# Kernel tuning notes

Measured on AMD Instinct MI355X. Metric: run time of the kernel, lower is better.

Reference implementation:

```python
import jax, jax.numpy as jnp
import numpy as np

LEAK = 0.01   # nn.LeakyReLU default negative_slope
EPS = 1e-5    # BatchNorm eps

D, H, W = 32, 480, 480
N = 200000
CIN, COUT = 64, 128


def _neighbor_table(z, y, x, order, sorted_flat, offsets):
    # For each kernel offset, index of the active voxel at (z+dz, y+dy, x+dx), or -1.
    n = z.shape[0]
    tabs = []
    for dz, dy, dx in offsets:
        nz, ny, nx = z + dz, y + dy, x + dx
        valid = (nz >= 0) & (nz < D) & (ny >= 0) & (ny < H) & (nx >= 0) & (nx < W)
        nflat = (nz * H + ny) * W + nx
        pos = np.searchsorted(sorted_flat, nflat).clip(0, n - 1)
        found = valid & (sorted_flat[pos] == nflat)
        tabs.append(np.where(found, order[pos], -1).astype(np.int32))
    return np.stack(tabs)  # [9, N]


def setup_inputs() -> dict:
    rng = np.random.default_rng(0)
    flat = rng.choice(D * H * W, N, replace=False).astype(np.int64)
    z = flat // (H * W)
    y = (flat // W) % H
    x = flat % W
    order = np.argsort(flat)
    sorted_flat = flat[order]
    off133 = [(0, dy, dx) for dy in (-1, 0, 1) for dx in (-1, 0, 1)]  # kernel (1,3,3)
    off313 = [(dz, 0, dx) for dz in (-1, 0, 1) for dx in (-1, 0, 1)]  # kernel (3,1,3)
    nbr133 = jnp.asarray(_neighbor_table(z, y, x, order, sorted_flat, off133))
    nbr313 = jnp.asarray(_neighbor_table(z, y, x, order, sorted_flat, off313))

    key = jax.random.key(0)
    ks = jax.random.split(key, 14)
    feats = jax.random.normal(ks[0], (N, CIN), jnp.float32)
    # SubMConv3d weights, flattened kernel volume first: [9, Cin, Cout]
    W00 = jax.random.normal(ks[1], (9, CIN, COUT), jnp.float32) * 0.05   # conv0_0 (1,3,3)
    W01 = jax.random.normal(ks[2], (9, COUT, COUT), jnp.float32) * 0.05  # conv0_1 (3,1,3)
    W10 = jax.random.normal(ks[3], (9, CIN, COUT), jnp.float32) * 0.05   # conv1_0 (3,1,3)
    W11 = jax.random.normal(ks[4], (9, COUT, COUT), jnp.float32) * 0.05  # conv1_1 (1,3,3)

    def bn_params(k):
        k1, k2, k3, k4 = jax.random.split(k, 4)
        gamma = 1.0 + 0.1 * jax.random.normal(k1, (COUT,), jnp.float32)
        beta = 0.1 * jax.random.normal(k2, (COUT,), jnp.float32)
        mean = 0.1 * jax.random.normal(k3, (COUT,), jnp.float32)
        var = jax.random.uniform(k4, (COUT,), jnp.float32, 0.5, 1.5)
        return jnp.stack([gamma, beta, mean, var])  # [4, Cout]

    return {
        'feats': feats,
        'W00': W00, 'W01': W01, 'W10': W10, 'W11': W11,
        'bn00': bn_params(ks[5]), 'bn01': bn_params(ks[6]),
        'bn10': bn_params(ks[7]), 'bn11': bn_params(ks[8]),
        'nbr133': nbr133, 'nbr313': nbr313,
    }


def _subm_conv(f, nbr, Wk):
    # Rulebook gather-matmul-accumulate: out[n] = sum_k f[nbr[k, n]] @ Wk[k]
    out = jnp.zeros((f.shape[0], Wk.shape[2]), f.dtype)
    for k in range(Wk.shape[0]):  # 9 fixed kernel offsets
        idx = nbr[k]
        valid = idx >= 0
        g = jnp.where(valid[:, None], f[jnp.where(valid, idx, 0)], 0.0)
        out = out + g @ Wk[k]
    return out


def _act_bn(x, p):
    # LeakyReLU then BatchNorm (eval: running stats), matching forward order
    x = jnp.where(x >= 0, x, LEAK * x)
    scale = p[0] * jax.lax.rsqrt(p[3] + EPS)
    return (x - p[2]) * scale + p[1]


def reference(feats, W00, W01, W10, W11, bn00, bn01, bn10, bn11, nbr133, nbr313):
    shortcut = _act_bn(_subm_conv(feats, nbr133, W00), bn00)
    shortcut = _act_bn(_subm_conv(shortcut, nbr313, W01), bn01)
    res = _act_bn(_subm_conv(feats, nbr313, W10), bn10)
    res = _act_bn(_subm_conv(res, nbr133, W11), bn11)
    return res + shortcut
```

## Files before the change

kernel.cpp:

```cpp
#include <hip/hip_runtime.h>
#include <hip/hip_bf16.h>

#define LEAK 0.01f
#define BN_EPS 1e-5f
#define CAP_P 8192

using frag_b16 = __attribute__((ext_vector_type(8))) short;
using f32x4    = __attribute__((ext_vector_type(4))) float;

union U4F { uint4 u; frag_b16 f; };

__device__ __forceinline__ float bf2f(unsigned short u) {
    union { unsigned int i; float f; } v;
    v.i = ((unsigned int)u) << 16;
    return v.f;
}

__device__ __forceinline__ unsigned short f2bf(float f) {
    union { float f; unsigned int i; } v;
    v.f = f;
    unsigned int u = v.i;
    return (unsigned short)((u + 0x7fffu + ((u >> 16) & 1u)) >> 16);
}

__device__ __forceinline__ unsigned int pk_bf16(float lo, float hi) {
    __hip_bfloat162 h = __float22bfloat162_rn(make_float2(lo, hi));
    union { __hip_bfloat162 h; unsigned int u; } c;
    c.h = h;
    return c.u;
}

__global__ __launch_bounds__(256) void transpose_all(
    const float* __restrict__ w0, const float* __restrict__ w1,
    const float* __restrict__ w2, const float* __restrict__ w3,
    const float* __restrict__ b0, const float* __restrict__ b1,
    const float* __restrict__ b2, const float* __restrict__ b3,
    unsigned short* __restrict__ o0, unsigned short* __restrict__ o1,
    unsigned short* __restrict__ o2, unsigned short* __restrict__ o3,
    float* __restrict__ scsh) {
    const int t64 = 9 * 64 * 128, t128 = 9 * 128 * 128;
    int i = blockIdx.x * 256 + threadIdx.x;
    const float* w; unsigned short* o; int cin;
    if (i < t64)                        { w = w0; o = o0; cin = 64; }
    else if ((i -= t64) < t128)         { w = w1; o = o1; cin = 128; }
    else if ((i -= t128) < t64)         { w = w2; o = o2; cin = 64; }
    else if ((i -= t64) < t128)         { w = w3; o = o3; cin = 128; }
    else if ((i -= t128) < 512) {
        int conv = i >> 7, c = i & 127;
        const float* bn = (conv == 0) ? b0 : (conv == 1) ? b1 : (conv == 2) ? b2 : b3;
        float s = bn[c] * rsqrtf(bn[384 + c] + BN_EPS);
        scsh[conv * 256 + c] = s;
        scsh[conv * 256 + 128 + c] = bn[128 + c] - bn[256 + c] * s;
        return;
    }
    else return;
    int co = i & 127;
    int rest = i >> 7;
    int ci = rest % cin;
    int k = rest / cin;
    o[((size_t)k * 128 + co) * cin + ci] = f2bf(w[i]);
}

__global__ __launch_bounds__(256) void feats_to_bf16(
    const float* __restrict__ f, unsigned short* __restrict__ o, int total8) {
    int i = blockIdx.x * 256 + threadIdx.x;
    if (i >= total8) return;
    const float4* p4 = (const float4*)(f + (size_t)i * 8);
    float4 a = p4[0], b = p4[1];
    uint4 u;
    u.x = pk_bf16(a.x, a.y); u.y = pk_bf16(a.z, a.w);
    u.z = pk_bf16(b.x, b.y); u.w = pk_bf16(b.z, b.w);
    ((uint4*)o)[i] = u;
}

__global__ __launch_bounds__(256) void rules_count(
    const int* __restrict__ nbrA, const int* __restrict__ nbrB,
    int N, int NB, int* __restrict__ blockCnt) {
    __shared__ int cnts[16][4];
    const int tid = threadIdx.x, lane = tid & 63, wave = tid >> 6;
    const int n = blockIdx.x * 256 + tid;
    #pragma unroll
    for (int c = 0; c < 16; ++c) {
        const int* nb = (c < 8) ? nbrA : nbrB;
        int j = c & 7;
        int k = j + (j >= 4);
        int v = (n < N) ? nb[(size_t)k * N + n] : -1;
        unsigned long long m = __ballot(v >= 0);
        if (lane == 0) cnts[c][wave] = __popcll(m);
    }
    __syncthreads();
    if (tid < 16)
        blockCnt[tid * NB + blockIdx.x] =
            cnts[tid][0] + cnts[tid][1] + cnts[tid][2] + cnts[tid][3];
}

__global__ __launch_bounds__(1024) void rules_scan(
    const int* __restrict__ blockCnt, int NB,
    int* __restrict__ blockBase, int* __restrict__ meta) {
    const int lane = threadIdx.x & 63, w = threadIdx.x >> 6;
    int running = 0;
    for (int base = 0; base < NB; base += 64) {
        int i = base + lane;
        int v = (i < NB) ? blockCnt[w * NB + i] : 0;
        int s = v;
        #pragma unroll
        for (int d = 1; d < 64; d <<= 1) {
            int t = __shfl_up(s, d);
            if (lane >= d) s += t;
        }
        if (i < NB) blockBase[w * NB + i] = running + s - v;
        running += __shfl(s, 63);
    }
    if (lane == 0) meta[w] = running;
}

__global__ __launch_bounds__(256) void rules_fill(
    const int* __restrict__ nbrA, const int* __restrict__ nbrB,
    int N, int NB, const int* __restrict__ blockBase,
    int* __restrict__ pairsAll,
    int* __restrict__ ptabA, int* __restrict__ ptabB,
    uint4* __restrict__ pakA, uint4* __restrict__ pakB) {
    __shared__ int wcnt[16][4];
    __shared__ int wpre[16][4];
    const int tid = threadIdx.x, lane = tid & 63, wave = tid >> 6;
    const int n = blockIdx.x * 256 + tid;
    int vv[16], rk[16];
    #pragma unroll
    for (int c = 0; c < 16; ++c) {
        const int* nb = (c < 8) ? nbrA : nbrB;
        int j = c & 7;
        int k = j + (j >= 4);
        int v = (n < N) ? nb[(size_t)k * N + n] : -1;
        vv[c] = v;
        unsigned long long m = __ballot(v >= 0);
        rk[c] = (int)__popcll(m & ((1ull << lane) - 1ull));
        if (lane == 0) wcnt[c][wave] = (int)__popcll(m);
    }
    __syncthreads();
    if (tid < 16) {
        int s = 0;
        #pragma unroll
        for (int w = 0; w < 4; ++w) { wpre[tid][w] = s; s += wcnt[tid][w]; }
    }
    __syncthreads();
    if (n < N) {
        unsigned long long la0 = ~0ull, la1 = ~0ull, lb0 = ~0ull, lb1 = ~0ull;
        int na = 0, nbp = 0;
        #pragma unroll
        for (int c = 0; c < 16; ++c) {
            int j = c & 7;
            int idx = -1;
            if (vv[c] >= 0) {
                idx = blockBase[c * NB + blockIdx.x] + wpre[c][wave] + rk[c];
                if (idx < CAP_P) pairsAll[c * CAP_P + idx] = vv[c];
                else idx = -1;
            }
            if (c < 8) { if (ptabA) ptabA[(size_t)n * 8 + j] = idx; }
            else       { if (ptabB) ptabB[(size_t)n * 8 + j] = idx; }
            if (idx >= 0) {
                unsigned e = ((unsigned)j << 13) | (unsigned)idx;
                if (e != 0xFFFFu) {
                    if (c < 8) {
                        int s = (na & 3) * 16;
                        unsigned long long m = 0xFFFFull << s;
                        unsigned long long ev = (unsigned long long)e << s;
                        if (na < 4) la0 = (la0 & ~m) | ev; else la1 = (la1 & ~m) | ev;
                        ++na;
                    } else {
                        int s = (nbp & 3) * 16;
                        unsigned long long m = 0xFFFFull << s;
                        unsigned long long ev = (unsigned long long)e << s;
                        if (nbp < 4) lb0 = (lb0 & ~m) | ev; else lb1 = (lb1 & ~m) | ev;
                        ++nbp;
                    }
                }
            }
        }
        if (pakA) pakA[n] = make_uint4((unsigned)la0, (unsigned)(la0 >> 32),
                                       (unsigned)la1, (unsigned)(la1 >> 32));
        if (pakB) pakB[n] = make_uint4((unsigned)lb0, (unsigned)(lb0 >> 32),
                                       (unsigned)lb1, (unsigned)(lb1 >> 32));
    }
}


__device__ __forceinline__ void merge_gather4(
    uint4 pk, const unsigned short* __restrict__ contrib, int cOff, f32x4 (&acc)[4]) {
    if (pk.x == 0xFFFFFFFFu) return;
    unsigned long long lo = ((unsigned long long)pk.y << 32) | pk.x;
    unsigned long long hi = ((unsigned long long)pk.w << 32) | pk.z;
    #pragma unroll 1
    for (int t = 0; t < 8; ++t) {
        unsigned v = (unsigned)(((t < 4) ? lo : hi) >> ((t & 3) << 4)) & 0xFFFFu;
        if (v == 0xFFFFu) break;
        const unsigned short* cr =
            contrib + ((size_t)(v >> 13) * CAP_P + (v & 0x1FFFu)) * 128 + cOff;
        #pragma unroll
        for (int ni = 0; ni < 4; ++ni) {
            uint2 g = *(const uint2*)(cr + ni * 16);
            acc[ni][0] += bf2f((unsigned short)(g.x & 0xffffu));
            acc[ni][1] += bf2f((unsigned short)(g.x >> 16));
            acc[ni][2] += bf2f((unsigned short)(g.y & 0xffffu));
            acc[ni][3] += bf2f((unsigned short)(g.y >> 16));
        }
    }
}

template <int CIN, bool IN_F32>
__global__ __launch_bounds__(256) void pairs_fused(
    const void* __restrict__ finA, const void* __restrict__ finB,
    const int*  __restrict__ pairsAll,
    const int*  __restrict__ meta,
    const unsigned short* __restrict__ wtA,
    const unsigned short* __restrict__ wtB,
    unsigned short* __restrict__ contribLo,
    unsigned short* __restrict__ contribHi,
    int pairXor) {
    const int job = blockIdx.y;
    const int j = job & 7, k = j + (j >= 4);
    const bool second = job >= 8;
    const void* fin = second ? finB : finA;
    const unsigned short* wk = (second ? wtB : wtA) + (size_t)k * 128 * CIN;
    unsigned short* ctb = (second ? contribHi : contribLo) + (size_t)j * CAP_P * 128;
    const int pidx = job ^ pairXor;
    const int* pairs = pairsAll + (size_t)pidx * CAP_P;
    const int cnt = min(meta[pidx], CAP_P);
    const int wave = threadIdx.x >> 6, lane = threadIdx.x & 63;
    const int l16 = lane & 15, quad = lane >> 4;
    const int pbase = (blockIdx.x * 4 + wave) * 16;
    if (pbase >= cnt) return;
    const int p = pbase + l16;
    const int inrow = (p < cnt) ? pairs[p] : -1;

    U4F uIn[CIN / 32];
    #pragma unroll
    for (int c = 0; c < CIN / 32; ++c) {
        uIn[c].u = make_uint4(0u, 0u, 0u, 0u);
        if (inrow >= 0) {
            if (IN_F32) {
                const float* fp = (const float*)fin;
                const float4* p4 = (const float4*)(fp + (size_t)inrow * CIN + c * 32 + quad * 8);
                float4 a = p4[0], b = p4[1];
                uIn[c].u.x = pk_bf16(a.x, a.y); uIn[c].u.y = pk_bf16(a.z, a.w);
                uIn[c].u.z = pk_bf16(b.x, b.y); uIn[c].u.w = pk_bf16(b.z, b.w);
            } else {
                uIn[c].u = *(const uint4*)((const unsigned short*)fin + (size_t)inrow * CIN + c * 32 + quad * 8);
            }
        }
    }

    f32x4 acc[8] = {};
    #pragma unroll
    for (int c = 0; c < CIN / 32; ++c) {
        frag_b16 bfr = uIn[c].f;
        #pragma unroll
        for (int ni = 0; ni < 8; ++ni) {
            frag_b16 afr = *(const frag_b16*)(wk + (size_t)(ni * 16 + l16) * CIN + c * 32 + quad * 8);
            acc[ni] = __builtin_amdgcn_mfma_f32_16x16x32_bf16(afr, bfr, acc[ni], 0, 0, 0);
        }
    }
    if (p < cnt) {
        unsigned short* cr = ctb + (size_t)p * 128 + quad * 4;
        #pragma unroll
        for (int ni = 0; ni < 8; ++ni) {
            uint2 o;
            o.x = pk_bf16(acc[ni][0], acc[ni][1]);
            o.y = pk_bf16(acc[ni][2], acc[ni][3]);
            *(uint2*)(cr + ni * 16) = o;
        }
    }
}

template <bool IN_F32>
__global__ __launch_bounds__(256) void convK1(
    const void* __restrict__ feats_,
    const unsigned short* __restrict__ wt00,
    const unsigned short* __restrict__ wt10,
    const uint4* __restrict__ pakA,
    const uint4* __restrict__ pakB,
    const unsigned short* __restrict__ contribLo,
    const unsigned short* __restrict__ contribHi,
    const float* __restrict__ scsh,
    unsigned short* __restrict__ s1,
    unsigned short* __restrict__ r1,
    int N) {
    constexpr int CIN = 64, SEGS = 8;
    __shared__ unsigned short ldsS[128 * CIN];
    __shared__ unsigned short ldsR[128 * CIN];
    const int tid = threadIdx.x, lane = tid & 63, wave = tid >> 6;
    const int waveM = wave >> 1, waveN = wave & 1;
    const int l16 = lane & 15, quad = lane >> 4;
    const int n0 = blockIdx.x * 64;
    {
        const unsigned short* wS = wt00 + (size_t)4 * 128 * CIN;
        const unsigned short* wR = wt10 + (size_t)4 * 128 * CIN;
        #pragma unroll
        for (int g = 0; g < (128 * SEGS) / 256; ++g) {
            int idx = g * 256 + tid;
            int row = idx / SEGS, seg = idx % SEGS;
            int dst = row * CIN + ((seg ^ (row & 7)) << 3);
            *(uint4*)(ldsS + dst) = *(const uint4*)(wS + row * CIN + seg * 8);
            *(uint4*)(ldsR + dst) = *(const uint4*)(wR + row * CIN + seg * 8);
        }
    }

    U4F bF[2][2];
    uint4 pA[2], pB[2];
    #pragma unroll
    for (int mi = 0; mi < 2; ++mi) {
        int n = n0 + waveM * 32 + mi * 16 + l16;
        pA[mi] = make_uint4(~0u, ~0u, ~0u, ~0u);
        pB[mi] = pA[mi];
        #pragma unroll
        for (int c = 0; c < 2; ++c) bF[c][mi].u = make_uint4(0u, 0u, 0u, 0u);
        if (n < N) {
            if (IN_F32) {
                const float* fp = (const float*)feats_;
                #pragma unroll
                for (int c = 0; c < 2; ++c) {
                    const float4* p4 = (const float4*)(fp + (size_t)n * 64 + c * 32 + quad * 8);
                    float4 a = p4[0], b = p4[1];
                    bF[c][mi].u.x = pk_bf16(a.x, a.y); bF[c][mi].u.y = pk_bf16(a.z, a.w);
                    bF[c][mi].u.z = pk_bf16(b.x, b.y); bF[c][mi].u.w = pk_bf16(b.z, b.w);
                }
            } else {
                #pragma unroll
                for (int c = 0; c < 2; ++c)
                    bF[c][mi].u = *(const uint4*)((const unsigned short*)feats_ + (size_t)n * 64 + c * 32 + quad * 8);
            }
            pA[mi] = pakA[n];
            pB[mi] = pakB[n];
        }
    }
    __syncthreads();

    f32x4 accS[2][4] = {}, accR[2][4] = {};
    #pragma unroll
    for (int c = 0; c < 2; ++c) {
        #pragma unroll
        for (int ni = 0; ni < 4; ++ni) {
            int off = (waveN * 64 + ni * 16 + l16) * CIN + ((((c << 2) + quad) ^ (l16 & 7)) << 3);
            frag_b16 aS = *(const frag_b16*)(ldsS + off);
            frag_b16 aR = *(const frag_b16*)(ldsR + off);
            #pragma unroll
            for (int mi = 0; mi < 2; ++mi) {
                accS[mi][ni] = __builtin_amdgcn_mfma_f32_16x16x32_bf16(aS, bF[c][mi].f, accS[mi][ni], 0, 0, 0);
                accR[mi][ni] = __builtin_amdgcn_mfma_f32_16x16x32_bf16(aR, bF[c][mi].f, accR[mi][ni], 0, 0, 0);
            }
        }
    }

    const int cOff = waveN * 64 + quad * 4;
    #pragma unroll
    for (int mi = 0; mi < 2; ++mi) {
        int n = n0 + waveM * 32 + mi * 16 + l16;
        if (n >= N) continue;
        merge_gather4(pA[mi], contribLo, cOff, accS[mi]);
        merge_gather4(pB[mi], contribHi, cOff, accR[mi]);
        #pragma unroll
        for (int ni = 0; ni < 4; ++ni) {
            int c = cOff + ni * 16;
            f32x4 scS = *(const f32x4*)(scsh + c);
            f32x4 shS = *(const f32x4*)(scsh + 128 + c);
            f32x4 scR = *(const f32x4*)(scsh + 512 + c);
            f32x4 shR = *(const f32x4*)(scsh + 640 + c);
            float vs[4], vr[4];
            #pragma unroll
            for (int r = 0; r < 4; ++r) {
                float xs = accS[mi][ni][r];
                xs = (xs >= 0.0f) ? xs : LEAK * xs;
                vs[r] = xs * scS[r] + shS[r];
                float xr = accR[mi][ni][r];
                xr = (xr >= 0.0f) ? xr : LEAK * xr;
                vr[r] = xr * scR[r] + shR[r];
            }
            uint2 oS, oR;
            oS.x = pk_bf16(vs[0], vs[1]); oS.y = pk_bf16(vs[2], vs[3]);
            oR.x = pk_bf16(vr[0], vr[1]); oR.y = pk_bf16(vr[2], vr[3]);
            *(uint2*)(s1 + (size_t)n * 128 + c) = oS;
            *(uint2*)(r1 + (size_t)n * 128 + c) = oR;
        }
    }
}

__global__ __launch_bounds__(256) void convK2(
    const unsigned short* __restrict__ s1,
    const unsigned short* __restrict__ r1,
    const unsigned short* __restrict__ wt01,
    const unsigned short* __restrict__ wt11,
    const uint4* __restrict__ pakB,
    const uint4* __restrict__ pakA,
    const unsigned short* __restrict__ contribLo,
    const unsigned short* __restrict__ contribHi,
    const float* __restrict__ scsh,
    float* __restrict__ out, int N) {
    constexpr int CIN = 128, SEGS = 16;
    __shared__ unsigned short ldsS[128 * CIN];
    __shared__ unsigned short ldsR[128 * CIN];
    const int tid = threadIdx.x, lane = tid & 63, wave = tid >> 6;
    const int waveM = wave >> 1, waveN = wave & 1;
    const int l16 = lane & 15, quad = lane >> 4;
    const int n0 = blockIdx.x * 64;
    {
        const unsigned short* wS = wt01 + (size_t)4 * 128 * CIN;
        const unsigned short* wR = wt11 + (size_t)4 * 128 * CIN;
        #pragma unroll
        for (int g = 0; g < (128 * SEGS) / 256; ++g) {
            int idx = g * 256 + tid;
            int row = idx >> 4, seg = idx & 15;
            int dst = row * CIN + ((seg ^ (row & 7)) << 3);
            *(uint4*)(ldsS + dst) = *(const uint4*)(wS + row * CIN + seg * 8);
            *(uint4*)(ldsR + dst) = *(const uint4*)(wR + row * CIN + seg * 8);
        }
    }

    U4F bS[4][2], bR[4][2];
    uint4 pS[2], pR[2];
    #pragma unroll
    for (int mi = 0; mi < 2; ++mi) {
        int n = n0 + waveM * 32 + mi * 16 + l16;
        pS[mi] = make_uint4(~0u, ~0u, ~0u, ~0u);
        pR[mi] = pS[mi];
        #pragma unroll
        for (int c = 0; c < 4; ++c) {
            bS[c][mi].u = make_uint4(0u, 0u, 0u, 0u);
            bR[c][mi].u = bS[c][mi].u;
        }
        if (n < N) {
            #pragma unroll
            for (int c = 0; c < 4; ++c) {
                bS[c][mi].u = *(const uint4*)(s1 + (size_t)n * 128 + c * 32 + quad * 8);
                bR[c][mi].u = *(const uint4*)(r1 + (size_t)n * 128 + c * 32 + quad * 8);
            }
            pS[mi] = pakB[n];
            pR[mi] = pakA[n];
        }
    }
    __syncthreads();

    f32x4 accS[2][4] = {}, accR[2][4] = {};
    #pragma unroll
    for (int c = 0; c < 4; ++c) {
        #pragma unroll
        for (int ni = 0; ni < 4; ++ni) {
            int off = (waveN * 64 + ni * 16 + l16) * CIN + ((((c << 2) + quad) ^ (l16 & 7)) << 3);
            frag_b16 aS = *(const frag_b16*)(ldsS + off);
            frag_b16 aR = *(const frag_b16*)(ldsR + off);
            #pragma unroll
            for (int mi = 0; mi < 2; ++mi) {
                accS[mi][ni] = __builtin_amdgcn_mfma_f32_16x16x32_bf16(aS, bS[c][mi].f, accS[mi][ni], 0, 0, 0);
                accR[mi][ni] = __builtin_amdgcn_mfma_f32_16x16x32_bf16(aR, bR[c][mi].f, accR[mi][ni], 0, 0, 0);
            }
        }
    }

    const int cOff = waveN * 64 + quad * 4;
    #pragma unroll
    for (int mi = 0; mi < 2; ++mi) {
        int n = n0 + waveM * 32 + mi * 16 + l16;
        if (n >= N) continue;
        merge_gather4(pS[mi], contribLo, cOff, accS[mi]);
        merge_gather4(pR[mi], contribHi, cOff, accR[mi]);
        #pragma unroll
        for (int ni = 0; ni < 4; ++ni) {
            int c = cOff + ni * 16;
            f32x4 sc1 = *(const f32x4*)(scsh + 256 + c);
            f32x4 sh1 = *(const f32x4*)(scsh + 384 + c);
            f32x4 sc3 = *(const f32x4*)(scsh + 768 + c);
            f32x4 sh3 = *(const f32x4*)(scsh + 896 + c);
            f32x4 o;
            #pragma unroll
            for (int r = 0; r < 4; ++r) {
                float xs = accS[mi][ni][r];
                xs = (xs >= 0.0f) ? xs : LEAK * xs;
                xs = xs * sc1[r] + sh1[r];
                float xr = accR[mi][ni][r];
                xr = (xr >= 0.0f) ? xr : LEAK * xr;
                xr = xr * sc3[r] + sh3[r];
                o[r] = xr + xs;
            }
            *(f32x4*)(out + (size_t)n * 128 + c) = o;
        }
    }
}


template <int CIN, bool IN_F32>
__global__ __launch_bounds__(256) void pairs_gemm2(
    const void* __restrict__ fin_,
    const int*  __restrict__ pairsT,
    const int*  __restrict__ metaT,
    const unsigned short* __restrict__ wt,
    unsigned short* __restrict__ contrib) {
    const int j = blockIdx.y;
    const int k = j + (j >= 4);
    const int cnt = min(metaT[j], CAP_P);
    const int wave = threadIdx.x >> 6, lane = threadIdx.x & 63;
    const int base = (blockIdx.x * 4 + wave) * 16;
    if (base >= cnt) return;
    const int l16 = lane & 15, quad = lane >> 4;
    const int p = base + l16;
    const int inrow = (p < cnt) ? pairsT[j * CAP_P + p] : -1;
    const unsigned short* wk = wt + (size_t)k * 128 * CIN;

    f32x4 acc[8] = {};
    #pragma unroll
    for (int c = 0; c < CIN / 32; ++c) {
        U4F u;
        u.u = make_uint4(0u, 0u, 0u, 0u);
        if (inrow >= 0) {
            if (IN_F32) {
                const float* fin = (const float*)fin_;
                const float4* p4 = (const float4*)(fin + (size_t)inrow * CIN + c * 32 + quad * 8);
                float4 a = p4[0], b = p4[1];
                u.u.x = pk_bf16(a.x, a.y); u.u.y = pk_bf16(a.z, a.w);
                u.u.z = pk_bf16(b.x, b.y); u.u.w = pk_bf16(b.z, b.w);
            } else {
                u.u = *(const uint4*)((const unsigned short*)fin_ + (size_t)inrow * CIN + c * 32 + quad * 8);
            }
        }
        frag_b16 af = u.f;
        #pragma unroll
        for (int ni = 0; ni < 8; ++ni) {
            frag_b16 bf = *(const frag_b16*)(wk + (ni * 16 + l16) * CIN + c * 32 + quad * 8);
            acc[ni] = __builtin_amdgcn_mfma_f32_16x16x32_bf16(af, bf, acc[ni], 0, 0, 0);
        }
    }
    unsigned short* cj = contrib + ((size_t)j * CAP_P + base) * 128;
    #pragma unroll
    for (int r = 0; r < 4; ++r) {
        int row = quad * 4 + r;
        #pragma unroll
        for (int ni = 0; ni < 8; ++ni)
            cj[(size_t)row * 128 + ni * 16 + l16] = f2bf(acc[ni][r]);
    }
}

template <int CIN, bool IN_F32, bool OUT_BF16, int ADDMODE>
__global__ __launch_bounds__(256, 4) void conv_center3(
    const void* __restrict__ fin_,
    const unsigned short* __restrict__ wt,
    const int*  __restrict__ ptabT,
    const unsigned short* __restrict__ contrib,
    const float* __restrict__ bn,
    const unsigned short* __restrict__ addbf,
    void* __restrict__ out_,
    int N) {
    const int tid = threadIdx.x;
    const int lane = tid & 63;
    const int wave = tid >> 6;
    const int waveM = wave >> 1, waveN = wave & 1;
    const int l16 = lane & 15, quad = lane >> 4;
    const int n0 = blockIdx.x * 64;
    const unsigned short* wc = wt + (size_t)4 * 128 * CIN;

    f32x4 acc[2][4] = {};
    #pragma unroll
    for (int c = 0; c < CIN / 32; ++c) {
        frag_b16 bf[4], af[2];
        #pragma unroll
        for (int ni = 0; ni < 4; ++ni)
            bf[ni] = *(const frag_b16*)(wc + (waveN * 64 + ni * 16 + l16) * CIN + c * 32 + quad * 8);
        #pragma unroll
        for (int mi = 0; mi < 2; ++mi) {
            int n = n0 + waveM * 32 + mi * 16 + l16;
            U4F u;
            u.u = make_uint4(0u, 0u, 0u, 0u);
            if (n < N) {
                if (IN_F32) {
                    const float* fin = (const float*)fin_;
                    const float4* p4 = (const float4*)(fin + (size_t)n * CIN + c * 32 + quad * 8);
                    float4 a = p4[0], b = p4[1];
                    u.u.x = pk_bf16(a.x, a.y); u.u.y = pk_bf16(a.z, a.w);
                    u.u.z = pk_bf16(b.x, b.y); u.u.w = pk_bf16(b.z, b.w);
                } else {
                    u.u = *(const uint4*)((const unsigned short*)fin_ + (size_t)n * CIN + c * 32 + quad * 8);
                }
            }
            af[mi] = u.f;
        }
        #pragma unroll
        for (int mi = 0; mi < 2; ++mi)
            #pragma unroll
            for (int ni = 0; ni < 4; ++ni)
                acc[mi][ni] = __builtin_amdgcn_mfma_f32_16x16x32_bf16(af[mi], bf[ni], acc[mi][ni], 0, 0, 0);
    }

    float sc[4], sh[4];
    int col[4];
    #pragma unroll
    for (int ni = 0; ni < 4; ++ni) {
        int c = waveN * 64 + ni * 16 + l16;
        col[ni] = c;
        float s = bn[c] * rsqrtf(bn[384 + c] + BN_EPS);
        sc[ni] = s;
        sh[ni] = bn[128 + c] - bn[256 + c] * s;
    }
    #pragma unroll
    for (int mi = 0; mi < 2; ++mi) {
        int rbase = n0 + waveM * 32 + mi * 16 + quad * 4;
        #pragma unroll
        for (int r = 0; r < 4; ++r) {
            int n = rbase + r;
            if (n < N) {
                const int4* pt = (const int4*)(ptabT + (size_t)n * 8);
                int4 pa = pt[0], pb = pt[1];
                int pj[8] = {pa.x, pa.y, pa.z, pa.w, pb.x, pb.y, pb.z, pb.w};
                float m[4] = {0.f, 0.f, 0.f, 0.f};
                #pragma unroll
                for (int j = 0; j < 8; ++j) {
                    int pi = pj[j];
                    if (pi >= 0) {
                        const unsigned short* cr = contrib + ((size_t)j * CAP_P + pi) * 128;
                        #pragma unroll
                        for (int ni = 0; ni < 4; ++ni) m[ni] += bf2f(cr[col[ni]]);
                    }
                }
                float addv[4] = {0.f, 0.f, 0.f, 0.f};
                if (ADDMODE == 1) {
                    #pragma unroll
                    for (int ni = 0; ni < 4; ++ni)
                        addv[ni] = bf2f(addbf[(size_t)n * 128 + col[ni]]);
                } else if (ADDMODE == 2) {
                    #pragma unroll
                    for (int ni = 0; ni < 4; ++ni)
                        addv[ni] = ((const float*)out_)[(size_t)n * 128 + col[ni]];
                }
                #pragma unroll
                for (int ni = 0; ni < 4; ++ni) {
                    float x = acc[mi][ni][r] + m[ni];
                    x = (x >= 0.0f) ? x : LEAK * x;
                    x = x * sc[ni] + sh[ni];
                    x += addv[ni];
                    if (OUT_BF16)
                        ((unsigned short*)out_)[(size_t)n * 128 + col[ni]] = f2bf(x);
                    else
                        ((float*)out_)[(size_t)n * 128 + col[ni]] = x;
                }
            }
        }
    }
}

template <int CIN, bool IN_F32, bool OUT_F32, bool ADD>
__global__ __launch_bounds__(256) void conv_mfma(
    const void*  __restrict__ fin_,
    const int*   __restrict__ nbr,
    const unsigned short* __restrict__ wt,
    const float* __restrict__ bn,
    const float* __restrict__ addsrc,
    void*        __restrict__ out_,
    int N) {
    constexpr int SEGS = CIN / 8;
    constexpr int RPP = 256 / SEGS;
    constexpr int PASSES = 128 / RPP;
    __shared__ unsigned short ldsA[128 * CIN];
    __shared__ unsigned short ldsW[128 * CIN];
    const int tid = threadIdx.x;
    const int lane = tid & 63;
    const int wave = tid >> 6;
    const int waveM = wave >> 1, waveN = wave & 1;
    const int l16 = lane & 15, quad = lane >> 4;
    const int n0 = blockIdx.x * 128;
    const int srow = tid / SEGS, sseg = tid % SEGS;
    f32x4 acc[4][4] = {};
    for (int k = 0; k < 9; ++k) {
        if (k) __syncthreads();
        #pragma unroll
        for (int p = 0; p < PASSES; ++p) {
            int r = p * RPP + srow;
            int n = n0 + r;
            int idx = (n < N) ? nbr[(size_t)k * N + n] : -1;
            uint4 v = make_uint4(0u, 0u, 0u, 0u);
            if (IN_F32) {
                const float* fin = (const float*)fin_;
                float4 a = make_float4(0.f, 0.f, 0.f, 0.f);
                float4 b = make_float4(0.f, 0.f, 0.f, 0.f);
                if (idx >= 0) {
                    const float4* p4 = (const float4*)(fin + (size_t)idx * CIN) + sseg * 2;
                    a = p4[0]; b = p4[1];
                }
                v.x = pk_bf16(a.x, a.y); v.y = pk_bf16(a.z, a.w);
                v.z = pk_bf16(b.x, b.y); v.w = pk_bf16(b.z, b.w);
            } else {
                const unsigned short* fin = (const unsigned short*)fin_;
                if (idx >= 0) v = *((const uint4*)(fin + (size_t)idx * CIN) + sseg);
            }
            *(uint4*)(ldsA + r * CIN + ((sseg ^ (r & 7)) << 3)) = v;
        }
        const unsigned short* wk = wt + (size_t)k * 128 * CIN;
        #pragma unroll
        for (int p = 0; p < PASSES; ++p) {
            int r = p * RPP + srow;
            *(uint4*)(ldsW + r * CIN + ((sseg ^ (r & 7)) << 3)) =
                *((const uint4*)(wk + r * CIN) + sseg);
        }
        __syncthreads();
        #pragma unroll
        for (int c = 0; c < CIN / 32; ++c) {
            frag_b16 af[4], bf[4];
            #pragma unroll
            for (int i = 0; i < 4; ++i) {
                int seg = (c * 4 + quad) ^ (l16 & 7);
                af[i] = *(const frag_b16*)(ldsA + (waveM * 64 + i * 16 + l16) * CIN + (seg << 3));
                bf[i] = *(const frag_b16*)(ldsW + (waveN * 64 + i * 16 + l16) * CIN + (seg << 3));
            }
            #pragma unroll
            for (int mi = 0; mi < 4; ++mi)
                #pragma unroll
                for (int ni = 0; ni < 4; ++ni)
                    acc[mi][ni] = __builtin_amdgcn_mfma_f32_16x16x32_bf16(af[mi], bf[ni], acc[mi][ni], 0, 0, 0);
        }
    }
    float sc[4], sh[4];
    int col[4];
    #pragma unroll
    for (int ni = 0; ni < 4; ++ni) {
        int c = waveN * 64 + ni * 16 + l16;
        col[ni] = c;
        float s = bn[c] * rsqrtf(bn[384 + c] + BN_EPS);
        sc[ni] = s;
        sh[ni] = bn[128 + c] - bn[256 + c] * s;
    }
    #pragma unroll
    for (int mi = 0; mi < 4; ++mi) {
        int rbase = n0 + waveM * 64 + mi * 16 + quad * 4;
        #pragma unroll
        for (int r = 0; r < 4; ++r) {
            int n = rbase + r;
            if (n < N) {
                #pragma unroll
                for (int ni = 0; ni < 4; ++ni) {
                    float x = acc[mi][ni][r];
                    x = (x >= 0.0f) ? x : LEAK * x;
                    x = x * sc[ni] + sh[ni];
                    if (ADD) x += addsrc[(size_t)n * 128 + col[ni]];
                    if (OUT_F32) ((float*)out_)[(size_t)n * 128 + col[ni]] = x;
                    else ((unsigned short*)out_)[(size_t)n * 128 + col[ni]] = f2bf(x);
                }
            }
        }
    }
}

extern "C" void kernel_launch(void* const* d_in, const int* in_sizes, int n_in,
                              void* d_out, int out_size, void* d_ws, size_t ws_size,
                              hipStream_t stream) {
    const float* feats = (const float*)d_in[0];
    const float* W00 = (const float*)d_in[1];
    const float* W01 = (const float*)d_in[2];
    const float* W10 = (const float*)d_in[3];
    const float* W11 = (const float*)d_in[4];
    const float* bn00 = (const float*)d_in[5];
    const float* bn01 = (const float*)d_in[6];
    const float* bn10 = (const float*)d_in[7];
    const float* bn11 = (const float*)d_in[8];
    const int* nbr133 = (const int*)d_in[9];
    const int* nbr313 = (const int*)d_in[10];
    const int N = in_sizes[0] / 64;
    const int NB = (N + 255) / 256;

    char* ws = (char*)d_ws;
    size_t off = 0;
    auto alloc = [&](size_t bytes) -> char* {
        char* p = ws + off;
        off = (off + bytes + 255) & ~(size_t)255;
        return p;
    };
    unsigned short* bufA = (unsigned short*)alloc((size_t)N * 128 * 2);
    unsigned short* wt00 = (unsigned short*)alloc(9 * 128 * 64 * 2);
    unsigned short* wt01 = (unsigned short*)alloc(9 * 128 * 128 * 2);
    unsigned short* wt10 = (unsigned short*)alloc(9 * 128 * 64 * 2);
    unsigned short* wt11 = (unsigned short*)alloc(9 * 128 * 128 * 2);
    float* scsh = (float*)alloc(4 * 2 * 128 * 4);
    int* pairsAll = (int*)alloc((size_t)16 * CAP_P * 4);
    int* blockCnt = (int*)alloc((size_t)16 * NB * 4);
    int* blockBase = (int*)alloc((size_t)16 * NB * 4);
    int* meta = (int*)alloc(16 * 4);
    unsigned short* contribLo = (unsigned short*)alloc((size_t)8 * CAP_P * 128 * 2);
    const size_t offX = off;

    uint4* pakA = (uint4*)alloc((size_t)N * 16);
    uint4* pakB = (uint4*)alloc((size_t)N * 16);
    unsigned short* bufB = (unsigned short*)alloc((size_t)N * 128 * 2);
    unsigned short* contribHi = (unsigned short*)alloc((size_t)8 * CAP_P * 128 * 2);
    const size_t offFused = off;
    unsigned short* feats16 = (unsigned short*)alloc((size_t)N * 64 * 2);
    const size_t offFusedF16 = off;

    off = offX;
    int* ptab133 = (int*)alloc((size_t)N * 8 * 4);
    int* ptab313 = (int*)alloc((size_t)N * 8 * 4);
    const size_t offTierB = off;
    unsigned short* bufB_t = (unsigned short*)alloc((size_t)N * 128 * 2);
    const size_t offTierA = off;

    const bool fusedOk = (ws_size >= offFused);
    const bool useF16 = (ws_size >= offFusedF16);
    const bool tierA = (ws_size >= offTierA);
    const bool tierB = (ws_size >= offTierB);

    const int totalW = 2 * (9 * 64 * 128) + 2 * (9 * 128 * 128);
    hipLaunchKernelGGL(transpose_all, dim3((totalW + 512 + 255) / 256), dim3(256), 0, stream,
                       W00, W01, W10, W11, bn00, bn01, bn10, bn11,
                       wt00, wt01, wt10, wt11, scsh);

    float* outF = (float*)d_out;
    const int cblocks = (N + 63) / 64;

    if (fusedOk) {
        if (useF16) {
            const int total8 = N * 8;
            hipLaunchKernelGGL(feats_to_bf16, dim3((total8 + 255) / 256), dim3(256), 0, stream,
                               feats, feats16, total8);
        }
        hipLaunchKernelGGL(rules_count, dim3(NB), dim3(256), 0, stream,
                           nbr133, nbr313, N, NB, blockCnt);
        hipLaunchKernelGGL(rules_scan, dim3(1), dim3(1024), 0, stream,
                           blockCnt, NB, blockBase, meta);
        hipLaunchKernelGGL(rules_fill, dim3(NB), dim3(256), 0, stream,
                           nbr133, nbr313, N, NB, blockBase, pairsAll,
                           (int*)nullptr, (int*)nullptr, pakA, pakB);

        const dim3 pg(CAP_P / 64, 16);
        if (useF16) {
            hipLaunchKernelGGL((pairs_fused<64, false>), pg, dim3(256), 0, stream,
                               (const void*)feats16, (const void*)feats16, pairsAll, meta,
                               wt00, wt10, contribLo, contribHi, 0);
            hipLaunchKernelGGL((convK1<false>), dim3(cblocks), dim3(256), 0, stream,
                               (const void*)feats16, wt00, wt10, pakA, pakB,
                               contribLo, contribHi, scsh, bufA, bufB, N);
        } else {
            hipLaunchKernelGGL((pairs_fused<64, true>), pg, dim3(256), 0, stream,
                               (const void*)feats, (const void*)feats, pairsAll, meta,
                               wt00, wt10, contribLo, contribHi, 0);
            hipLaunchKernelGGL((convK1<true>), dim3(cblocks), dim3(256), 0, stream,
                               (const void*)feats, wt00, wt10, pakA, pakB,
                               contribLo, contribHi, scsh, bufA, bufB, N);
        }
        hipLaunchKernelGGL((pairs_fused<128, false>), pg, dim3(256), 0, stream,
                           (const void*)bufA, (const void*)bufB, pairsAll, meta,
                           wt01, wt11, contribLo, contribHi, 8);
        hipLaunchKernelGGL(convK2, dim3(cblocks), dim3(256), 0, stream,
                           bufA, bufB, wt01, wt11, pakB, pakA,
                           contribLo, contribHi, scsh, outF, N);
    } else if (tierA || tierB) {
        hipLaunchKernelGGL(rules_count, dim3(NB), dim3(256), 0, stream,
                           nbr133, nbr313, N, NB, blockCnt);
        hipLaunchKernelGGL(rules_scan, dim3(1), dim3(1024), 0, stream,
                           blockCnt, NB, blockBase, meta);
        hipLaunchKernelGGL(rules_fill, dim3(NB), dim3(256), 0, stream,
                           nbr133, nbr313, N, NB, blockBase, pairsAll,
                           ptab133, ptab313, (uint4*)nullptr, (uint4*)nullptr);

        const dim3 pg(CAP_P / 64, 8);
        const int* pairs133 = pairsAll;
        const int* pairs313 = pairsAll + 8 * CAP_P;
        const int* meta133 = meta;
        const int* meta313 = meta + 8;
        const unsigned short* nullbf = nullptr;

        hipLaunchKernelGGL((pairs_gemm2<64, true>), pg, dim3(256), 0, stream,
                           (const void*)feats, pairs133, meta133, wt00, contribLo);
        hipLaunchKernelGGL((conv_center3<64, true, true, 0>), dim3(cblocks), dim3(256), 0, stream,
                           (const void*)feats, wt00, ptab133, contribLo, bn00, nullbf, (void*)bufA, N);
        hipLaunchKernelGGL((pairs_gemm2<128, false>), pg, dim3(256), 0, stream,
                           (const void*)bufA, pairs313, meta313, wt01, contribLo);
        if (tierA)
            hipLaunchKernelGGL((conv_center3<128, false, true, 0>), dim3(cblocks), dim3(256), 0, stream,
                               (const void*)bufA, wt01, ptab313, contribLo, bn01, nullbf, (void*)bufB_t, N);
        else
            hipLaunchKernelGGL((conv_center3<128, false, false, 0>), dim3(cblocks), dim3(256), 0, stream,
                               (const void*)bufA, wt01, ptab313, contribLo, bn01, nullbf, (void*)outF, N);
        hipLaunchKernelGGL((pairs_gemm2<64, true>), pg, dim3(256), 0, stream,
                           (const void*)feats, pairs313, meta313, wt10, contribLo);
        hipLaunchKernelGGL((conv_center3<64, true, true, 0>), dim3(cblocks), dim3(256), 0, stream,
                           (const void*)feats, wt10, ptab313, contribLo, bn10, nullbf, (void*)bufA, N);
        hipLaunchKernelGGL((pairs_gemm2<128, false>), pg, dim3(256), 0, stream,
                           (const void*)bufA, pairs133, meta133, wt11, contribLo);
        if (tierA)
            hipLaunchKernelGGL((conv_center3<128, false, false, 1>), dim3(cblocks), dim3(256), 0, stream,
                               (const void*)bufA, wt11, ptab133, contribLo, bn11, bufB_t, (void*)outF, N);
        else
            hipLaunchKernelGGL((conv_center3<128, false, false, 2>), dim3(cblocks), dim3(256), 0, stream,
                               (const void*)bufA, wt11, ptab133, contribLo, bn11, nullbf, (void*)outF, N);
    } else {
        const int blocks = (N + 127) / 128;
        hipLaunchKernelGGL((conv_mfma<64, true, false, false>), dim3(blocks), dim3(256), 0, stream,
                           (const void*)feats, nbr133, wt00, bn00, (const float*)nullptr, (void*)bufA, N);
        hipLaunchKernelGGL((conv_mfma<128, false, true, false>), dim3(blocks), dim3(256), 0, stream,
                           (const void*)bufA, nbr313, wt01, bn01, (const float*)nullptr, (void*)outF, N);
        hipLaunchKernelGGL((conv_mfma<64, true, false, false>), dim3(blocks), dim3(256), 0, stream,
                           (const void*)feats, nbr313, wt10, bn10, (const float*)nullptr, (void*)bufA, N);
        hipLaunchKernelGGL((conv_mfma<128, false, true, true>), dim3(blocks), dim3(256), 0, stream,
                           (const void*)bufA, nbr133, wt11, bn11, outF, (void*)outF, N);
    }
}
```

Measured before the change: 394.1 us.

## Stage pair-GEMM weights in LDS and double conv block size

The pair GEMM kernel now loads each offset's weight slice into swizzled shared memory once per block and loops each wave over four 16-pair sub-tiles, instead of every wave reading weights straight from global memory. The grid shrinks by four in x to match. The centre conv kernels convK1/convK2 move to 512-thread blocks covering 128 rows, which halves the per-row cost of loading the shared weight tiles. The trade-off is more LDS per block for the pair kernel and less parallelism when pair counts are small.

Measured after the change: 371.3 us. -5.8%, faster.

```diff
diff --git a/kernel.cpp b/kernel.cpp
--- a/kernel.cpp
+++ b/kernel.cpp
@@ -207,7 +207,7 @@
 }
 
 template <int CIN, bool IN_F32>
-__global__ __launch_bounds__(256) void pairs_fused(
+__global__ __launch_bounds__(256) void pairs_fused2(
     const void* __restrict__ finA, const void* __restrict__ finB,
     const int*  __restrict__ pairsAll,
     const int*  __restrict__ meta,
@@ -216,63 +216,74 @@
     unsigned short* __restrict__ contribLo,
     unsigned short* __restrict__ contribHi,
     int pairXor) {
+    constexpr int SEGS = CIN / 8;
+    __shared__ unsigned short ldsW[128 * CIN];
     const int job = blockIdx.y;
     const int j = job & 7, k = j + (j >= 4);
     const bool second = job >= 8;
+    const int pidx = job ^ pairXor;
+    const int cnt = min(meta[pidx], CAP_P);
+    if ((int)blockIdx.x * 256 >= cnt) return;
     const void* fin = second ? finB : finA;
     const unsigned short* wk = (second ? wtB : wtA) + (size_t)k * 128 * CIN;
     unsigned short* ctb = (second ? contribHi : contribLo) + (size_t)j * CAP_P * 128;
-    const int pidx = job ^ pairXor;
     const int* pairs = pairsAll + (size_t)pidx * CAP_P;
-    const int cnt = min(meta[pidx], CAP_P);
-    const int wave = threadIdx.x >> 6, lane = threadIdx.x & 63;
+    const int tid = threadIdx.x, lane = tid & 63, wave = tid >> 6;
     const int l16 = lane & 15, quad = lane >> 4;
-    const int pbase = (blockIdx.x * 4 + wave) * 16;
-    if (pbase >= cnt) return;
-    const int p = pbase + l16;
-    const int inrow = (p < cnt) ? pairs[p] : -1;
-
-    U4F uIn[CIN / 32];
-    #pragma unroll
-    for (int c = 0; c < CIN / 32; ++c) {
-        uIn[c].u = make_uint4(0u, 0u, 0u, 0u);
-        if (inrow >= 0) {
-            if (IN_F32) {
-                const float* fp = (const float*)fin;
-                const float4* p4 = (const float4*)(fp + (size_t)inrow * CIN + c * 32 + quad * 8);
-                float4 a = p4[0], b = p4[1];
-                uIn[c].u.x = pk_bf16(a.x, a.y); uIn[c].u.y = pk_bf16(a.z, a.w);
-                uIn[c].u.z = pk_bf16(b.x, b.y); uIn[c].u.w = pk_bf16(b.z, b.w);
-            } else {
-                uIn[c].u = *(const uint4*)((const unsigned short*)fin + (size_t)inrow * CIN + c * 32 + quad * 8);
-            }
-        }
-    }
-
-    f32x4 acc[8] = {};
-    #pragma unroll
-    for (int c = 0; c < CIN / 32; ++c) {
-        frag_b16 bfr = uIn[c].f;
-        #pragma unroll
-        for (int ni = 0; ni < 8; ++ni) {
-            frag_b16 afr = *(const frag_b16*)(wk + (size_t)(ni * 16 + l16) * CIN + c * 32 + quad * 8);
-            acc[ni] = __builtin_amdgcn_mfma_f32_16x16x32_bf16(afr, bfr, acc[ni], 0, 0, 0);
-        }
-    }
-    if (p < cnt) {
-        unsigned short* cr = ctb + (size_t)p * 128 + quad * 4;
-        #pragma unroll
-        for (int ni = 0; ni < 8; ++ni) {
-            uint2 o;
-            o.x = pk_bf16(acc[ni][0], acc[ni][1]);
-            o.y = pk_bf16(acc[ni][2], acc[ni][3]);
-            *(uint2*)(cr + ni * 16) = o;
+    #pragma unroll
+    for (int g = 0; g < (128 * SEGS) / 256; ++g) {
+        int idx = g * 256 + tid;
+        int row = idx / SEGS, seg = idx % SEGS;
+        *(uint4*)(ldsW + row * CIN + ((seg ^ (row & 7)) << 3)) =
+            *(const uint4*)(wk + row * CIN + seg * 8);
+    }
+    __syncthreads();
+    const int p00 = blockIdx.x * 256 + wave * 64;
+    #pragma unroll 1
+    for (int sub = 0; sub < 4; ++sub) {
+        int base = p00 + sub * 16;
+        if (base >= cnt) break;
+        int p = base + l16;
+        int inrow = (p < cnt) ? pairs[p] : -1;
+        f32x4 acc[8] = {};
+        #pragma unroll
+        for (int c = 0; c < CIN / 32; ++c) {
+            U4F u;
+            u.u = make_uint4(0u, 0u, 0u, 0u);
+            if (inrow >= 0) {
+                if (IN_F32) {
+                    const float* fp = (const float*)fin;
+                    const float4* p4 = (const float4*)(fp + (size_t)inrow * CIN + c * 32 + quad * 8);
+                    float4 a = p4[0], b = p4[1];
+                    u.u.x = pk_bf16(a.x, a.y); u.u.y = pk_bf16(a.z, a.w);
+                    u.u.z = pk_bf16(b.x, b.y); u.u.w = pk_bf16(b.z, b.w);
+                } else {
+                    u.u = *(const uint4*)((const unsigned short*)fin + (size_t)inrow * CIN + c * 32 + quad * 8);
+                }
+            }
+            frag_b16 bfr = u.f;
+            #pragma unroll
+            for (int ni = 0; ni < 8; ++ni) {
+                int off = (ni * 16 + l16) * CIN + ((((c << 2) + quad) ^ (l16 & 7)) << 3);
+                frag_b16 afr = *(const frag_b16*)(ldsW + off);
+                acc[ni] = __builtin_amdgcn_mfma_f32_16x16x32_bf16(afr, bfr, acc[ni], 0, 0, 0);
+            }
+        }
+        if (p < cnt) {
+            unsigned short* cr = ctb + (size_t)p * 128 + quad * 4;
+            #pragma unroll
+            for (int ni = 0; ni < 8; ++ni) {
+                uint2 o;
+                o.x = pk_bf16(acc[ni][0], acc[ni][1]);
+                o.y = pk_bf16(acc[ni][2], acc[ni][3]);
+                *(uint2*)(cr + ni * 16) = o;
+            }
         }
     }
 }
 
 template <bool IN_F32>
-__global__ __launch_bounds__(256) void convK1(
+__global__ __launch_bounds__(512) void convK1(
     const void* __restrict__ feats_,
     const unsigned short* __restrict__ wt00,
     const unsigned short* __restrict__ wt10,
@@ -290,13 +301,13 @@
     const int tid = threadIdx.x, lane = tid & 63, wave = tid >> 6;
     const int waveM = wave >> 1, waveN = wave & 1;
     const int l16 = lane & 15, quad = lane >> 4;
-    const int n0 = blockIdx.x * 64;
+    const int n0 = blockIdx.x * 128;
     {
         const unsigned short* wS = wt00 + (size_t)4 * 128 * CIN;
         const unsigned short* wR = wt10 + (size_t)4 * 128 * CIN;
         #pragma unroll
-        for (int g = 0; g < (128 * SEGS) / 256; ++g) {
-            int idx = g * 256 + tid;
+        for (int g = 0; g < (128 * SEGS) / 512; ++g) {
+            int idx = g * 512 + tid;
             int row = idx / SEGS, seg = idx % SEGS;
             int dst = row * CIN + ((seg ^ (row & 7)) << 3);
             *(uint4*)(ldsS + dst) = *(const uint4*)(wS + row * CIN + seg * 8);
@@ -383,7 +394,7 @@
     }
 }
 
-__global__ __launch_bounds__(256) void convK2(
+__global__ __launch_bounds__(512) void convK2(
     const unsigned short* __restrict__ s1,
     const unsigned short* __restrict__ r1,
     const unsigned short* __restrict__ wt01,
@@ -400,13 +411,13 @@
     const int tid = threadIdx.x, lane = tid & 63, wave = tid >> 6;
     const int waveM = wave >> 1, waveN = wave & 1;
     const int l16 = lane & 15, quad = lane >> 4;
-    const int n0 = blockIdx.x * 64;
+    const int n0 = blockIdx.x * 128;
     {
         const unsigned short* wS = wt01 + (size_t)4 * 128 * CIN;
         const unsigned short* wR = wt11 + (size_t)4 * 128 * CIN;
         #pragma unroll
-        for (int g = 0; g < (128 * SEGS) / 256; ++g) {
-            int idx = g * 256 + tid;
+        for (int g = 0; g < (128 * SEGS) / 512; ++g) {
+            int idx = g * 512 + tid;
             int row = idx >> 4, seg = idx & 15;
             int dst = row * CIN + ((seg ^ (row & 7)) << 3);
             *(uint4*)(ldsS + dst) = *(const uint4*)(wS + row * CIN + seg * 8);
@@ -806,7 +817,7 @@
                        wt00, wt01, wt10, wt11, scsh);
 
     float* outF = (float*)d_out;
-    const int cblocks = (N + 63) / 64;
+    const int kblocks = (N + 127) / 128;
 
     if (fusedOk) {
         if (useF16) {
@@ -822,26 +833,26 @@
                            nbr133, nbr313, N, NB, blockBase, pairsAll,
                            (int*)nullptr, (int*)nullptr, pakA, pakB);
 
-        const dim3 pg(CAP_P / 64, 16);
+        const dim3 pg2(CAP_P / 256, 16);
         if (useF16) {
-            hipLaunchKernelGGL((pairs_fused<64, false>), pg, dim3(256), 0, stream,
+            hipLaunchKernelGGL((pairs_fused2<64, false>), pg2, dim3(256), 0, stream,
                                (const void*)feats16, (const void*)feats16, pairsAll, meta,
                                wt00, wt10, contribLo, contribHi, 0);
-            hipLaunchKernelGGL((convK1<false>), dim3(cblocks), dim3(256), 0, stream,
+            hipLaunchKernelGGL((convK1<false>), dim3(kblocks), dim3(512), 0, stream,
                                (const void*)feats16, wt00, wt10, pakA, pakB,
                                contribLo, contribHi, scsh, bufA, bufB, N);
         } else {
-            hipLaunchKernelGGL((pairs_fused<64, true>), pg, dim3(256), 0, stream,
+            hipLaunchKernelGGL((pairs_fused2<64, true>), pg2, dim3(256), 0, stream,
                                (const void*)feats, (const void*)feats, pairsAll, meta,
                                wt00, wt10, contribLo, contribHi, 0);
-            hipLaunchKernelGGL((convK1<true>), dim3(cblocks), dim3(256), 0, stream,
+            hipLaunchKernelGGL((convK1<true>), dim3(kblocks), dim3(512), 0, stream,
                                (const void*)feats, wt00, wt10, pakA, pakB,
                                contribLo, contribHi, scsh, bufA, bufB, N);
         }
-        hipLaunchKernelGGL((pairs_fused<128, false>), pg, dim3(256), 0, stream,
+        hipLaunchKernelGGL((pairs_fused2<128, false>), pg2, dim3(256), 0, stream,
                            (const void*)bufA, (const void*)bufB, pairsAll, meta,
                            wt01, wt11, contribLo, contribHi, 8);
-        hipLaunchKernelGGL(convK2, dim3(cblocks), dim3(256), 0, stream,
+        hipLaunchKernelGGL(convK2, dim3(kblocks), dim3(512), 0, stream,
                            bufA, bufB, wt01, wt11, pakB, pakA,
                            contribLo, contribHi, scsh, outF, N);
     } else if (tierA || tierB) {
@@ -859,6 +870,7 @@
         const int* meta133 = meta;
         const int* meta313 = meta + 8;
         const unsigned short* nullbf = nullptr;
+        const int cblocks = (N + 63) / 64;
 
         hipLaunchKernelGGL((pairs_gemm2<64, true>), pg, dim3(256), 0, stream,
                            (const void*)feats, pairs133, meta133, wt00, contribLo);
```
